# Kernel tuning notes

Hardware: AMD Instinct MI355X
Metric: run time of the kernel (lower is better)

The kernel has to match this reference:

```python
import jax, jax.numpy as jnp
import numpy as np


def setup_inputs() -> dict:
    key = jax.random.key(0)
    k_x, k_W, k_b, k_ids, k_w = jax.random.split(key, 5)
    N_ADAPTERS, D_OUT, D_IN = 32, 1024, 1024
    B, S = 2, 2048
    K = 8  # number of active adapters
    x = jax.random.normal(k_x, (B, S, D_IN), dtype=jnp.float32)
    W = jax.random.normal(k_W, (N_ADAPTERS, D_OUT, D_IN), dtype=jnp.float32)
    b = jax.random.normal(k_b, (N_ADAPTERS, D_OUT), dtype=jnp.float32)
    ids = jax.random.randint(k_ids, (K,), 0, N_ADAPTERS, dtype=jnp.int64)
    weights = jax.random.uniform(k_w, (K,), dtype=jnp.float32)
    return {"x": x, "W": W, "b": b, "ids": ids, "weights": weights}


def reference(x, W, b, ids, weights):
    # Original: out_i = Linear_{ids[i]}(x); output = sum_i weights[i] * out_i
    Wsel = W[ids]  # [k, o, d]  gather of selected adapter weights
    bsel = b[ids]  # [k, o]
    # Fused weighted mixture of k small GEMMs (same math as loop + weighted sum)
    out = jnp.einsum("k,kod,bsd->bso", weights, Wsel, x)
    out = out + jnp.einsum("k,ko->o", weights, bsel)
    return out
```

## Files before the change

kernel.cpp:

```cpp
#include <hip/hip_runtime.h>
#include <hip/hip_bf16.h>
#include <stdint.h>


typedef __attribute__((ext_vector_type(8))) short short8;
typedef __attribute__((ext_vector_type(4))) float float4v;

#define DIMK 1024
#define DIMN 1024
#define DIMM 4096

__device__ __forceinline__ unsigned short f2bf_rtn(float f) {
  union { float f; unsigned u; } v; v.f = f;
  unsigned u = v.u;
  return (unsigned short)((u + 0x7fffu + ((u >> 16) & 1u)) >> 16);
}

__global__ __launch_bounds__(256) void prep_kernel(
    const float* __restrict__ x, const float* __restrict__ W,
    const float* __restrict__ bia, const int* __restrict__ ids,
    const float* __restrict__ wts,
    unsigned short* __restrict__ xb, unsigned short* __restrict__ Wc,
    float* __restrict__ bc, int K)
{
  const int bid = blockIdx.x;
  if (bid < 1024) {
    const int t  = bid * 256 + threadIdx.x;
    const int o  = t >> 8;
    const int d4 = (t & 255) << 2;
    float ax = 0.f, ay = 0.f, az = 0.f, aw = 0.f;
    for (int k = 0; k < K; ++k) {
      const float wk = wts[k];
      const float4 w4 = *reinterpret_cast<const float4*>(
          &W[((size_t)ids[k] << 20) + ((size_t)o << 10) + d4]);
      ax += wk * w4.x; ay += wk * w4.y; az += wk * w4.z; aw += wk * w4.w;
    }
    ushort4 r;
    r.x = f2bf_rtn(ax); r.y = f2bf_rtn(ay); r.z = f2bf_rtn(az); r.w = f2bf_rtn(aw);
    *reinterpret_cast<ushort4*>(&Wc[(size_t)t << 2]) = r;
    if (t < DIMN) {
      float s = 0.f;
      for (int k = 0; k < K; ++k) s += wts[k] * bia[ids[k] * DIMN + t];
      bc[t] = s;
    }
  } else {
    const size_t t = (size_t)(bid - 1024) * 256 + threadIdx.x;
    const float4 v = *reinterpret_cast<const float4*>(&x[t << 2]);
    ushort4 r;
    r.x = f2bf_rtn(v.x); r.y = f2bf_rtn(v.y); r.z = f2bf_rtn(v.z); r.w = f2bf_rtn(v.w);
    *reinterpret_cast<ushort4*>(&xb[t << 2]) = r;
  }
}

__device__ __forceinline__ void load_lds16(const void* g, void* l) {
  __builtin_amdgcn_global_load_lds(
      (const __attribute__((address_space(1))) void*)g,
      (__attribute__((address_space(3))) void*)l, 16, 0, 0);
}

__global__ __launch_bounds__(256, 2) void gemm_kernel(
    const unsigned short* __restrict__ xb,
    const unsigned short* __restrict__ Wc,
    const float* __restrict__ bc,
    float* __restrict__ out)
{
  constexpr int BK = 64;
  __shared__ __align__(16) unsigned short As[64 * BK];
  __shared__ __align__(16) unsigned short Bs[128 * BK];

  const int tid  = threadIdx.x;
  const int wave = tid >> 6;
  const int lane = tid & 63;
  const int m0 = blockIdx.y * 64;
  const int n0 = blockIdx.x * 128;

  const int srow = lane >> 3;
  const int scol = (((lane & 7) ^ srow) << 3);
  const unsigned short* gA0 = xb + (size_t)(m0 + wave * 16 + srow) * DIMK + scol;
  const unsigned short* gA1 = gA0 + 8 * DIMK;
  const unsigned short* gB0 = Wc + (size_t)(n0 + wave * 32 + srow) * DIMK + scol;
  const unsigned short* gB1 = gB0 + 8 * DIMK;
  const unsigned short* gB2 = gB0 + 16 * DIMK;
  const unsigned short* gB3 = gB0 + 24 * DIMK;
  unsigned short* lA0 = &As[wave * 16 * BK];
  unsigned short* lA1 = lA0 + 8 * BK;
  unsigned short* lB0 = &Bs[wave * 32 * BK];
  unsigned short* lB1 = lB0 + 8 * BK;
  unsigned short* lB2 = lB0 + 16 * BK;
  unsigned short* lB3 = lB0 + 24 * BK;

  const int wm   = (wave >> 1) * 32;
  const int wn   = (wave & 1) * 64;
  const int quad = lane >> 4;
  const int r16  = lane & 15;
  const int rx   = r16 & 7;
  const int po0  = ((quad ^ rx) << 3);
  const int po1  = (((4 + quad) ^ rx) << 3);

  const float4v zero = {0.f, 0.f, 0.f, 0.f};
  float4v acc[2][4];
#pragma unroll
  for (int i = 0; i < 2; ++i)
#pragma unroll
    for (int j = 0; j < 4; ++j) acc[i][j] = zero;

  for (int k0 = 0; k0 < DIMK; k0 += BK) {
    load_lds16(gA0 + k0, lA0);
    load_lds16(gA1 + k0, lA1);
    load_lds16(gB0 + k0, lB0);
    load_lds16(gB1 + k0, lB1);
    load_lds16(gB2 + k0, lB2);
    load_lds16(gB3 + k0, lB3);
    __syncthreads();

#pragma unroll
    for (int s = 0; s < 2; ++s) {
      const int po = s ? po1 : po0;
      short8 af[2], bf[4];
#pragma unroll
      for (int mt = 0; mt < 2; ++mt)
        af[mt] = *reinterpret_cast<const short8*>(&As[(wm + mt * 16 + r16) * BK + po]);
#pragma unroll
      for (int nt = 0; nt < 4; ++nt)
        bf[nt] = *reinterpret_cast<const short8*>(&Bs[(wn + nt * 16 + r16) * BK + po]);
#pragma unroll
      for (int mt = 0; mt < 2; ++mt)
#pragma unroll
        for (int nt = 0; nt < 4; ++nt)
          acc[mt][nt] = __builtin_amdgcn_mfma_f32_16x16x32_bf16(af[mt], bf[nt], acc[mt][nt], 0, 0, 0);
    }
    __syncthreads();
  }

#pragma unroll
  for (int nt = 0; nt < 4; ++nt) {
    const int col = n0 + wn + nt * 16 + r16;
    const float bias = bc[col];
#pragma unroll
    for (int mt = 0; mt < 2; ++mt) {
      const int rbase = m0 + wm + mt * 16 + quad * 4;
#pragma unroll
      for (int r = 0; r < 4; ++r)
        out[(size_t)(rbase + r) * DIMN + col] = acc[mt][nt][r] + bias;
    }
  }
}

extern "C" void kernel_launch(void* const* d_in, const int* in_sizes, int n_in,
                              void* d_out, int out_size, void* d_ws, size_t ws_size,
                              hipStream_t stream) {
  const float* x   = (const float*)d_in[0];
  const float* W   = (const float*)d_in[1];
  const float* b   = (const float*)d_in[2];
  const int*   ids = (const int*)d_in[3];
  const float* wts = (const float*)d_in[4];
  float* out = (float*)d_out;
  const int K = in_sizes[3];

  unsigned short* xb = (unsigned short*)d_ws;
  unsigned short* Wc = (unsigned short*)((char*)d_ws + (8u << 20));
  float*          bc = (float*)((char*)d_ws + (10u << 20));

  prep_kernel<<<5120, 256, 0, stream>>>(x, W, b, ids, wts, xb, Wc, bc, K);
  dim3 grid(DIMN / 128, DIMM / 64);
  gemm_kernel<<<grid, 256, 0, stream>>>(xb, Wc, bc, out);
}
```

Baseline: 203.0 us.

## Double-buffer LDS and enlarge GEMM tile to 128x128, widen x conversion

The GEMM tile grows from 64x128 to 128x128, so each wave computes a 64x64 sub-tile with 16 accumulators, which raises MFMA work per loaded byte. The LDS buffers are now double-buffered so the async global-to-LDS load of the next K slice overlaps compute on the current one, leaving one barrier per slice. The x-to-bf16 conversion handles 8 floats per thread, so the prep grid shrinks. In exchange, register and LDS use go up (64 KB LDS, 64 accumulator floats per thread) and the 256-block GEMM grid may underfill the GPU's CUs.

```diff
diff --git a/kernel.cpp b/kernel.cpp
--- a/kernel.cpp
+++ b/kernel.cpp
@@ -45,10 +45,13 @@
     }
   } else {
     const size_t t = (size_t)(bid - 1024) * 256 + threadIdx.x;
-    const float4 v = *reinterpret_cast<const float4*>(&x[t << 2]);
-    ushort4 r;
-    r.x = f2bf_rtn(v.x); r.y = f2bf_rtn(v.y); r.z = f2bf_rtn(v.z); r.w = f2bf_rtn(v.w);
-    *reinterpret_cast<ushort4*>(&xb[t << 2]) = r;
+    const float4 v0 = *reinterpret_cast<const float4*>(&x[t << 3]);
+    const float4 v1 = *reinterpret_cast<const float4*>(&x[(t << 3) + 4]);
+    ushort4 r0, r1;
+    r0.x = f2bf_rtn(v0.x); r0.y = f2bf_rtn(v0.y); r0.z = f2bf_rtn(v0.z); r0.w = f2bf_rtn(v0.w);
+    r1.x = f2bf_rtn(v1.x); r1.y = f2bf_rtn(v1.y); r1.z = f2bf_rtn(v1.z); r1.w = f2bf_rtn(v1.w);
+    *reinterpret_cast<ushort4*>(&xb[t << 3]) = r0;
+    *reinterpret_cast<ushort4*>(&xb[(t << 3) + 4]) = r1;
   }
 }
 
@@ -58,38 +61,30 @@
       (__attribute__((address_space(3))) void*)l, 16, 0, 0);
 }
 
-__global__ __launch_bounds__(256, 2) void gemm_kernel(
+__global__ __launch_bounds__(256) void gemm_kernel(
     const unsigned short* __restrict__ xb,
     const unsigned short* __restrict__ Wc,
     const float* __restrict__ bc,
     float* __restrict__ out)
 {
   constexpr int BK = 64;
-  __shared__ __align__(16) unsigned short As[64 * BK];
-  __shared__ __align__(16) unsigned short Bs[128 * BK];
+  constexpr int BM = 128;
+  constexpr int BN = 128;
+  __shared__ __align__(16) unsigned short As[2][BM * BK];
+  __shared__ __align__(16) unsigned short Bs[2][BN * BK];
 
   const int tid  = threadIdx.x;
   const int wave = tid >> 6;
   const int lane = tid & 63;
-  const int m0 = blockIdx.y * 64;
-  const int n0 = blockIdx.x * 128;
+  const int m0 = blockIdx.y * BM;
+  const int n0 = blockIdx.x * BN;
 
   const int srow = lane >> 3;
   const int scol = (((lane & 7) ^ srow) << 3);
-  const unsigned short* gA0 = xb + (size_t)(m0 + wave * 16 + srow) * DIMK + scol;
-  const unsigned short* gA1 = gA0 + 8 * DIMK;
-  const unsigned short* gB0 = Wc + (size_t)(n0 + wave * 32 + srow) * DIMK + scol;
-  const unsigned short* gB1 = gB0 + 8 * DIMK;
-  const unsigned short* gB2 = gB0 + 16 * DIMK;
-  const unsigned short* gB3 = gB0 + 24 * DIMK;
-  unsigned short* lA0 = &As[wave * 16 * BK];
-  unsigned short* lA1 = lA0 + 8 * BK;
-  unsigned short* lB0 = &Bs[wave * 32 * BK];
-  unsigned short* lB1 = lB0 + 8 * BK;
-  unsigned short* lB2 = lB0 + 16 * BK;
-  unsigned short* lB3 = lB0 + 24 * BK;
+  const unsigned short* gA = xb + (size_t)(m0 + wave * 32 + srow) * DIMK + scol;
+  const unsigned short* gB = Wc + (size_t)(n0 + wave * 32 + srow) * DIMK + scol;
 
-  const int wm   = (wave >> 1) * 32;
+  const int wm   = (wave >> 1) * 64;
   const int wn   = (wave & 1) * 64;
   const int quad = lane >> 4;
   const int r16  = lane & 15;
@@ -98,46 +93,67 @@
   const int po1  = (((4 + quad) ^ rx) << 3);
 
   const float4v zero = {0.f, 0.f, 0.f, 0.f};
-  float4v acc[2][4];
+  float4v acc[4][4];
 #pragma unroll
-  for (int i = 0; i < 2; ++i)
+  for (int i = 0; i < 4; ++i)
 #pragma unroll
     for (int j = 0; j < 4; ++j) acc[i][j] = zero;
 
-  for (int k0 = 0; k0 < DIMK; k0 += BK) {
-    load_lds16(gA0 + k0, lA0);
-    load_lds16(gA1 + k0, lA1);
-    load_lds16(gB0 + k0, lB0);
-    load_lds16(gB1 + k0, lB1);
-    load_lds16(gB2 + k0, lB2);
-    load_lds16(gB3 + k0, lB3);
+#define STAGE(buf, k0)                                                         \
+  do {                                                                         \
+    _Pragma("unroll")                                                          \
+    for (int c = 0; c < 4; ++c) {                                              \
+      load_lds16(gA + (size_t)(k0) + (size_t)c * 8 * DIMK,                     \
+                 &As[buf][(wave * 32 + c * 8) * BK]);                          \
+      load_lds16(gB + (size_t)(k0) + (size_t)c * 8 * DIMK,                     \
+                 &Bs[buf][(wave * 32 + c * 8) * BK]);                          \
+    }                                                                          \
+  } while (0)
+
+#define COMPUTE(buf)                                                           \
+  do {                                                                         \
+    _Pragma("unroll")                                                          \
+    for (int s = 0; s < 2; ++s) {                                              \
+      const int po = s ? po1 : po0;                                            \
+      short8 af[4], bf[4];                                                     \
+      _Pragma("unroll")                                                        \
+      for (int mt = 0; mt < 4; ++mt)                                           \
+        af[mt] = *reinterpret_cast<const short8*>(                             \
+            &As[buf][(wm + mt * 16 + r16) * BK + po]);                         \
+      _Pragma("unroll")                                                        \
+      for (int nt = 0; nt < 4; ++nt)                                           \
+        bf[nt] = *reinterpret_cast<const short8*>(                             \
+            &Bs[buf][(wn + nt * 16 + r16) * BK + po]);                         \
+      _Pragma("unroll")                                                        \
+      for (int mt = 0; mt < 4; ++mt)                                           \
+        _Pragma("unroll")                                                      \
+        for (int nt = 0; nt < 4; ++nt)                                         \
+          acc[mt][nt] = __builtin_amdgcn_mfma_f32_16x16x32_bf16(               \
+              af[mt], bf[nt], acc[mt][nt], 0, 0, 0);                           \
+    }                                                                          \
+  } while (0)
+
+  STAGE(0, 0);
+  __syncthreads();
+
+  for (int t = 0; t < DIMK / BK; t += 2) {
+    STAGE(1, (t + 1) * BK);
+    COMPUTE(0);
     __syncthreads();
-
-#pragma unroll
-    for (int s = 0; s < 2; ++s) {
-      const int po = s ? po1 : po0;
-      short8 af[2], bf[4];
-#pragma unroll
-      for (int mt = 0; mt < 2; ++mt)
-        af[mt] = *reinterpret_cast<const short8*>(&As[(wm + mt * 16 + r16) * BK + po]);
-#pragma unroll
-      for (int nt = 0; nt < 4; ++nt)
-        bf[nt] = *reinterpret_cast<const short8*>(&Bs[(wn + nt * 16 + r16) * BK + po]);
-#pragma unroll
-      for (int mt = 0; mt < 2; ++mt)
-#pragma unroll
-        for (int nt = 0; nt < 4; ++nt)
-          acc[mt][nt] = __builtin_amdgcn_mfma_f32_16x16x32_bf16(af[mt], bf[nt], acc[mt][nt], 0, 0, 0);
-    }
+    if (t + 2 < DIMK / BK) STAGE(0, (t + 2) * BK);
+    COMPUTE(1);
     __syncthreads();
   }
+
+#undef STAGE
+#undef COMPUTE
 
 #pragma unroll
   for (int nt = 0; nt < 4; ++nt) {
     const int col = n0 + wn + nt * 16 + r16;
     const float bias = bc[col];
 #pragma unroll
-    for (int mt = 0; mt < 2; ++mt) {
+    for (int mt = 0; mt < 4; ++mt) {
       const int rbase = m0 + wm + mt * 16 + quad * 4;
 #pragma unroll
       for (int r = 0; r < 4; ++r)
@@ -161,7 +177,7 @@
   unsigned short* Wc = (unsigned short*)((char*)d_ws + (8u << 20));
   float*          bc = (float*)((char*)d_ws + (10u << 20));
 
-  prep_kernel<<<5120, 256, 0, stream>>>(x, W, b, ids, wts, xb, Wc, bc, K);
-  dim3 grid(DIMN / 128, DIMM / 64);
+  prep_kernel<<<3072, 256, 0, stream>>>(x, W, b, ids, wts, xb, Wc, bc, K);
+  dim3 grid(DIMN / 128, DIMM / 128);
   gemm_kernel<<<grid, 256, 0, stream>>>(xb, Wc, bc, out);
 }
```

After: 209.7 us. 3.3% more time.
